# Kernel tuning notes

Hardware: AMD Instinct MI355X
Metric: run time of the kernel (lower is better)

## Reference

```python
import jax, jax.numpy as jnp
import numpy as np

EPS = 1e-7  # keras backend epsilon

def setup_inputs() -> dict:
    key = jax.random.key(0)
    k1, k2, k3 = jax.random.split(key, 3)
    B, L, D, P = 16, 1024, 256, 20
    sent1 = jax.random.normal(k1, (B, L, D), dtype=jnp.float32)
    sent2 = jax.random.normal(k2, (B, L, D), dtype=jnp.float32)
    kernel = jax.random.normal(k3, (P, D), dtype=jnp.float32) * 0.1
    return {"sent1": sent1, "sent2": sent2, "kernel": kernel}

def reference(sent1, sent2, kernel):
    # token norms with keras-style clamping: sqrt(max(sum(x^2), eps))
    n1 = jnp.sqrt(jnp.maximum(jnp.sum(sent1 * sent1, axis=-1), EPS))  # [B,L1]
    n2 = jnp.sqrt(jnp.maximum(jnp.sum(sent2 * sent2, axis=-1), EPS))  # [B,L2]
    # all-pairs cosine matrix via matmul instead of broadcast-multiply-reduce
    dots = jnp.einsum('bld,bmd->blm', sent1, sent2)                    # [B,L1,L2]
    cos = dots / n1[:, :, None] / n2[:, None, :]
    # mean attentive vectors: cosine-weighted sum of sent2, normalized by row sum
    weighted = jnp.einsum('blm,bmd->bld', cos, sent2)                  # [B,L1,D]
    mav = weighted / (jnp.sum(cos, axis=-1, keepdims=True) + EPS)      # [B,L1,D]
    # perspective-weighted cosine between sent1*k and mav*k, fused without [B,L,P,D]
    k2 = kernel * kernel                                               # [P,D]
    num = jnp.einsum('bld,pd->blp', sent1 * mav, k2)                   # sum_d s1*mav*k^2
    nv1 = jnp.sqrt(jnp.maximum(jnp.einsum('bld,pd->blp', sent1 * sent1, k2), EPS))
    nv2 = jnp.sqrt(jnp.maximum(jnp.einsum('bld,pd->blp', mav * mav, k2), EPS))
    return num / nv1 / nv2                                             # [B,L1,P]
```

## Files before the change

### kernel.cpp

```cpp
#include <hip/hip_runtime.h>
#include <math.h>

#define EPS 1e-7f

constexpr int B = 16, L = 1024, D = 256, P = 20;
constexpr int LD = L * D;
constexpr int DD = D * D;

typedef __attribute__((ext_vector_type(8))) _Float16 f16x8;
typedef __attribute__((ext_vector_type(4))) float f32x4;


__device__ inline unsigned short f2h(float x) {
    _Float16 h = (_Float16)x;
    union { _Float16 h; unsigned short u; } c; c.h = h; return c.u;
}
__device__ inline float h2f(unsigned short u) {
    union { unsigned short u; _Float16 h; } c; c.u = u; return (float)c.h;
}

__global__ __launch_bounds__(256) void k_prep2(const float* __restrict__ s2,
                                               float* __restrict__ tp,
                                               unsigned short* __restrict__ CT) {
    __shared__ float tile[32][257];
    __shared__ float wiv[32];
    __shared__ float wsq[32];
    int tid = threadIdx.x;
    int b   = blockIdx.x >> 5, mt = blockIdx.x & 31;
    int m0  = mt * 32;
    {
        int r = tid >> 3, c0 = (tid & 7) * 32;
        const float* gp = s2 + (size_t)b * LD + (size_t)(m0 + r) * D + c0;
        float4 v[8];
#pragma unroll
        for (int q = 0; q < 8; ++q) v[q] = ((const float4*)gp)[q];
#pragma unroll
        for (int q = 0; q < 8; ++q) *(float4*)&tile[r][c0 + q * 4] = v[q];
    }
    __syncthreads();
    {
        int r = tid >> 3, seg = tid & 7;
        float s = 0.f;
#pragma unroll
        for (int k = 0; k < 32; ++k) { float v = tile[r][seg * 32 + k]; s += v * v; }
#pragma unroll
        for (int o = 4; o; o >>= 1) s += __shfl_down(s, o, 8);
        if (seg == 0) {
            float iv = 1.0f / sqrtf(fmaxf(s, EPS));
            wiv[r] = iv;
            wsq[r] = sqrtf(iv);
        }
    }
    __syncthreads();
    {
        int dc = tid;
        float tpart = 0.f;
        union { unsigned short us[32]; uint4 q[4]; } ph;
#pragma unroll
        for (int m = 0; m < 32; ++m) {
            float v = tile[m][dc];
            tpart += v * wiv[m];
            ph.us[m] = f2h(v * wsq[m]);
        }
        tp[(size_t)(mt * B + b) * D + dc] = tpart;
        size_t o = (size_t)b * LD + (size_t)dc * L + m0;
        *(uint4*)(CT + o)      = ph.q[0]; *(uint4*)(CT + o + 8)  = ph.q[1];
        *(uint4*)(CT + o + 16) = ph.q[2]; *(uint4*)(CT + o + 24) = ph.q[3];
    }
}

__global__ __launch_bounds__(256) void k_u(const float* __restrict__ s1,
                                           const float* __restrict__ tp,
                                           float* __restrict__ invU,
                                           unsigned short* __restrict__ s1f) {
    __shared__ float ts[D];
    int tid = threadIdx.x;
    {
        int b0 = (blockIdx.x * 4) >> 10;
        float acc = 0.f;
#pragma unroll
        for (int mc = 0; mc < 32; ++mc)
            acc += tp[(size_t)(mc * B + b0) * D + tid];
        ts[tid] = acc;
    }
    __syncthreads();

    int w = tid >> 6, lane = tid & 63;
    int row = blockIdx.x * 4 + w;
    int dg = lane & 15;

    float4 sv[4];
    float up = 0.f, sq = 0.f;
#pragma unroll
    for (int j = 0; j < 4; ++j) {
        sv[j] = *(const float4*)(s1 + (size_t)row * D + dg * 4 + j * 64);
        float4 tv = *(const float4*)(ts + dg * 4 + j * 64);
        up += sv[j].x * tv.x + sv[j].y * tv.y + sv[j].z * tv.z + sv[j].w * tv.w;
        sq += sv[j].x * sv[j].x + sv[j].y * sv[j].y + sv[j].z * sv[j].z + sv[j].w * sv[j].w;
    }
#pragma unroll
    for (int o = 8; o; o >>= 1) {
        up += __shfl_down(up, o, 16);
        sq += __shfl_down(sq, o, 16);
    }
    if (lane == 0) {
        float n1v = sqrtf(fmaxf(sq, EPS));
        invU[row] = 1.0f / (up + EPS * n1v);
    }
#pragma unroll
    for (int j = 0; j < 4; ++j) {
        ushort4 h4;
        h4.x = f2h(sv[j].x); h4.y = f2h(sv[j].y);
        h4.z = f2h(sv[j].z); h4.w = f2h(sv[j].w);
        *(ushort4*)(s1f + (size_t)row * D + dg * 4 + j * 64) = h4;
    }
}

__global__ __launch_bounds__(256) void k_gram_mfma(const unsigned short* __restrict__ CT,
                                                   float* __restrict__ Gp) {
    __shared__ short As[128 * 72];
    __shared__ short Bs[64 * 72];
    int tid  = threadIdx.x;
    int b    = blockIdx.x >> 5;
    int rem  = blockIdx.x & 31;
    int ti   = rem >> 4;
    int tj   = (rem >> 2) & 3;
    int kc   = rem & 3;
    int wave = tid >> 6, lane = tid & 63;
    int wr   = (wave >> 1) * 64, wcc = (wave & 1) * 32;
    int lr   = lane & 15, lq = lane >> 4;
    int arow = tid >> 1, ahalf = (tid & 1) * 32;
    int brow = tid >> 2, bq = (tid & 3) * 16;

    f32x4 acc[4][2];
#pragma unroll
    for (int i = 0; i < 4; ++i)
#pragma unroll
        for (int j = 0; j < 2; ++j) acc[i][j] = (f32x4){0.f, 0.f, 0.f, 0.f};

#pragma unroll 1
    for (int kb = 0; kb < 4; ++kb) {
        int koff = kc * 256 + kb * 64;
        __syncthreads();
        {
            const unsigned short* ga = CT + (size_t)b * LD + (size_t)(ti * 128 + arow) * L + koff + ahalf;
            uint4 a0 = ((const uint4*)ga)[0], a1 = ((const uint4*)ga)[1];
            uint4 a2 = ((const uint4*)ga)[2], a3 = ((const uint4*)ga)[3];
            const unsigned short* gb = CT + (size_t)b * LD + (size_t)(tj * 64 + brow) * L + koff + bq;
            uint4 b0 = ((const uint4*)gb)[0], b1 = ((const uint4*)gb)[1];
            short* la = &As[arow * 72 + ahalf];
            ((uint4*)la)[0] = a0; ((uint4*)la)[1] = a1;
            ((uint4*)la)[2] = a2; ((uint4*)la)[3] = a3;
            short* lb = &Bs[brow * 72 + bq];
            ((uint4*)lb)[0] = b0; ((uint4*)lb)[1] = b1;
        }
        __syncthreads();
#pragma unroll
        for (int ks = 0; ks < 2; ++ks) {
            f16x8 af[4], bfr[2];
#pragma unroll
            for (int i = 0; i < 4; ++i)
                af[i] = *(const f16x8*)&As[(wr + i * 16 + lr) * 72 + ks * 32 + lq * 8];
#pragma unroll
            for (int j = 0; j < 2; ++j)
                bfr[j] = *(const f16x8*)&Bs[(wcc + j * 16 + lr) * 72 + ks * 32 + lq * 8];
#pragma unroll
            for (int i = 0; i < 4; ++i)
#pragma unroll
                for (int j = 0; j < 2; ++j)
                    acc[i][j] = __builtin_amdgcn_mfma_f32_16x16x32_f16(af[i], bfr[j], acc[i][j], 0, 0, 0);
        }
    }
    float* gout = Gp + ((size_t)(kc * B + b)) * DD;
#pragma unroll
    for (int i = 0; i < 4; ++i)
#pragma unroll
        for (int r = 0; r < 4; ++r) {
            int row = ti * 128 + wr + i * 16 + lq * 4 + r;
#pragma unroll
            for (int j = 0; j < 2; ++j)
                gout[(size_t)row * D + tj * 64 + wcc + j * 16 + lr] = acc[i][j][r];
        }
}

__global__ __launch_bounds__(256) void k_reduceG(const float* __restrict__ Gp,
                                                 unsigned short* __restrict__ Gf) {
    size_t i = ((size_t)blockIdx.x * 256 + threadIdx.x) * 4;
    float4 s = *(const float4*)(Gp + i);
#pragma unroll
    for (int kc = 1; kc < 4; ++kc) {
        float4 a = *(const float4*)(Gp + (size_t)kc * B * DD + i);
        s.x += a.x; s.y += a.y; s.z += a.z; s.w += a.w;
    }
    ushort4 h4;
    h4.x = f2h(s.x); h4.y = f2h(s.y); h4.z = f2h(s.z); h4.w = f2h(s.w);
    *(ushort4*)(Gf + i) = h4;
}

__global__ __launch_bounds__(256) void k_mav_mfma(const unsigned short* __restrict__ s1f,
                                                  const unsigned short* __restrict__ Gf,
                                                  unsigned short* __restrict__ mavh) {
    __shared__ short As[64 * 72];
    __shared__ short Bs[128 * 72];
    int tid  = threadIdx.x;
    int b    = blockIdx.x >> 5;
    int rem  = blockIdx.x & 31;
    int lt   = rem >> 1, nt = rem & 1;
    int l0   = lt * 64, n0 = nt * 128;
    int wave = tid >> 6, lane = tid & 63;
    int wn   = wave * 32;
    int lr   = lane & 15, lq = lane >> 4;
    int arow = tid >> 2, aq = (tid & 3) * 16;
    int brow = tid >> 1, bhalf = (tid & 1) * 32;

    f32x4 acc[4][2];
#pragma unroll
    for (int i = 0; i < 4; ++i)
#pragma unroll
        for (int j = 0; j < 2; ++j) acc[i][j] = (f32x4){0.f, 0.f, 0.f, 0.f};

#pragma unroll 1
    for (int kb = 0; kb < 4; ++kb) {
        int koff = kb * 64;
        __syncthreads();
        {
            const unsigned short* ga = s1f + (size_t)(b * L + l0 + arow) * D + koff + aq;
            uint4 a0 = ((const uint4*)ga)[0], a1 = ((const uint4*)ga)[1];
            const unsigned short* gb = Gf + (size_t)b * DD + (size_t)(n0 + brow) * D + koff + bhalf;
            uint4 b0 = ((const uint4*)gb)[0], b1 = ((const uint4*)gb)[1];
            uint4 b2 = ((const uint4*)gb)[2], b3 = ((const uint4*)gb)[3];
            short* la = &As[arow * 72 + aq];
            ((uint4*)la)[0] = a0; ((uint4*)la)[1] = a1;
            short* lb = &Bs[brow * 72 + bhalf];
            ((uint4*)lb)[0] = b0; ((uint4*)lb)[1] = b1;
            ((uint4*)lb)[2] = b2; ((uint4*)lb)[3] = b3;
        }
        __syncthreads();
#pragma unroll
        for (int ks = 0; ks < 2; ++ks) {
            f16x8 af[4], bfr[2];
#pragma unroll
            for (int i = 0; i < 4; ++i)
                af[i] = *(const f16x8*)&As[(i * 16 + lr) * 72 + ks * 32 + lq * 8];
#pragma unroll
            for (int j = 0; j < 2; ++j)
                bfr[j] = *(const f16x8*)&Bs[(wn + j * 16 + lr) * 72 + ks * 32 + lq * 8];
#pragma unroll
            for (int i = 0; i < 4; ++i)
#pragma unroll
                for (int j = 0; j < 2; ++j)
                    acc[i][j] = __builtin_amdgcn_mfma_f32_16x16x32_f16(af[i], bfr[j], acc[i][j], 0, 0, 0);
        }
    }
#pragma unroll
    for (int i = 0; i < 4; ++i)
#pragma unroll
        for (int r = 0; r < 4; ++r) {
            int l = l0 + i * 16 + lq * 4 + r;
#pragma unroll
            for (int j = 0; j < 2; ++j)
                mavh[(size_t)(b * L + l) * D + n0 + wn + j * 16 + lr] = f2h(acc[i][j][r]);
        }
}

__global__ __launch_bounds__(256) void k_out(const unsigned short* __restrict__ s1f,
                                             const unsigned short* __restrict__ mavh,
                                             const float* __restrict__ invU,
                                             const float* __restrict__ kern,
                                             float* __restrict__ out) {
    __shared__ float k2s[P * D];
    int tid = threadIdx.x;
#pragma unroll
    for (int p = 0; p < P; ++p) {
        float v = kern[p * D + tid];
        k2s[p * D + tid] = v * v;
    }
    __syncthreads();

    int w = tid >> 6, lane = tid & 63;
    int row = blockIdx.x * 4 + w;
    int dg = lane & 15, ps = lane >> 4;

    float4 sm[4], ss[4], mm[4];
#pragma unroll
    for (int j = 0; j < 4; ++j) {
        ushort4 h4 = *(const ushort4*)(s1f + (size_t)row * D + dg * 4 + j * 64);
        ushort4 m4 = *(const ushort4*)(mavh + (size_t)row * D + dg * 4 + j * 64);
        float4 sv, mv;
        sv.x = h2f(h4.x); sv.y = h2f(h4.y); sv.z = h2f(h4.z); sv.w = h2f(h4.w);
        mv.x = h2f(m4.x); mv.y = h2f(m4.y); mv.z = h2f(m4.z); mv.w = h2f(m4.w);
        sm[j].x = sv.x * mv.x; sm[j].y = sv.y * mv.y; sm[j].z = sv.z * mv.z; sm[j].w = sv.w * mv.w;
        ss[j].x = sv.x * sv.x; ss[j].y = sv.y * sv.y; ss[j].z = sv.z * sv.z; ss[j].w = sv.w * sv.w;
        mm[j].x = mv.x * mv.x; mm[j].y = mv.y * mv.y; mm[j].z = mv.z * mv.z; mm[j].w = mv.w * mv.w;
    }
    float sgn = (invU[row] < 0.f) ? -1.f : 1.f;
#pragma unroll
    for (int tI = 0; tI < 5; ++tI) {
        int p = ps + tI * 4;
        float na = 0.f, nb = 0.f, nc = 0.f;
#pragma unroll
        for (int j = 0; j < 4; ++j) {
            float4 kv = *(const float4*)&k2s[p * D + j * 64 + dg * 4];
            na += sm[j].x * kv.x + sm[j].y * kv.y + sm[j].z * kv.z + sm[j].w * kv.w;
            nb += ss[j].x * kv.x + ss[j].y * kv.y + ss[j].z * kv.z + ss[j].w * kv.w;
            nc += mm[j].x * kv.x + mm[j].y * kv.y + mm[j].z * kv.z + mm[j].w * kv.w;
        }
#pragma unroll
        for (int o = 8; o; o >>= 1) {
            na += __shfl_down(na, o, 16);
            nb += __shfl_down(nb, o, 16);
            nc += __shfl_down(nc, o, 16);
        }
        if (dg == 0) {
            out[(size_t)row * P + p] = sgn * na * rsqrtf(fmaxf(nb, EPS)) *
                                       rsqrtf(fmaxf(nc, EPS));
        }
    }
}

extern "C" void kernel_launch(void* const* d_in, const int* in_sizes, int n_in,
                              void* d_out, int out_size, void* d_ws, size_t ws_size,
                              hipStream_t stream) {
    const float* s1   = (const float*)d_in[0];
    const float* s2   = (const float*)d_in[1];
    const float* kern = (const float*)d_in[2];
    float* out = (float*)d_out;
    float* ws  = (float*)d_ws;

    float* tp   = ws;
    float* invU = ws + 131072;
    unsigned short* s1f  = (unsigned short*)(ws + 147456);
    unsigned short* CT   = (unsigned short*)(ws + 2244608);
    unsigned short* Gf   = (unsigned short*)(ws + 4341760);
    float* Gp   = ws + 4866048;
    unsigned short* mavh = (unsigned short*)(ws + 9060352);

    k_prep2<<<512, 256, 0, stream>>>(s2, tp, CT);
    k_u<<<4096, 256, 0, stream>>>(s1, tp, invU, s1f);
    k_gram_mfma<<<512, 256, 0, stream>>>(CT, Gp);
    k_reduceG<<<1024, 256, 0, stream>>>(Gp, Gf);
    k_mav_mfma<<<512, 256, 0, stream>>>(s1f, Gf, mavh);
    k_out<<<4096, 256, 0, stream>>>(s1f, mavh, invU, kern, out);
}
```

Measured before the change: 127.5 us.

## Fuse gram split-K reduction in LDS and merge mav, norm and output kernels

The Gram kernel is retiled to 32x32 output tiles, with its split-K done across the four waves and reduced in shared memory, so the fp32 partial buffer and the separate reduce kernel go away. The s1 conversion and norm kernel, the mav MFMA kernel and the output kernel are merged into one 512-thread block per 64 rows. That block keeps the s1 half-precision tile and the mav tile in LDS and never writes them to global memory. This cuts six launches to three and removes large intermediate traffic, at the cost of heavy LDS use per block and only 256 blocks in the fused kernel, which may limit occupancy.

```diff
diff --git a/kernel.cpp b/kernel.cpp
--- a/kernel.cpp
+++ b/kernel.cpp
@@ -69,251 +69,216 @@
     }
 }
 
-__global__ __launch_bounds__(256) void k_u(const float* __restrict__ s1,
-                                           const float* __restrict__ tp,
-                                           float* __restrict__ invU,
-                                           unsigned short* __restrict__ s1f) {
-    __shared__ float ts[D];
-    int tid = threadIdx.x;
-    {
-        int b0 = (blockIdx.x * 4) >> 10;
-        float acc = 0.f;
-#pragma unroll
-        for (int mc = 0; mc < 32; ++mc)
-            acc += tp[(size_t)(mc * B + b0) * D + tid];
-        ts[tid] = acc;
-    }
-    __syncthreads();
-
-    int w = tid >> 6, lane = tid & 63;
-    int row = blockIdx.x * 4 + w;
-    int dg = lane & 15;
-
-    float4 sv[4];
-    float up = 0.f, sq = 0.f;
-#pragma unroll
-    for (int j = 0; j < 4; ++j) {
-        sv[j] = *(const float4*)(s1 + (size_t)row * D + dg * 4 + j * 64);
-        float4 tv = *(const float4*)(ts + dg * 4 + j * 64);
-        up += sv[j].x * tv.x + sv[j].y * tv.y + sv[j].z * tv.z + sv[j].w * tv.w;
-        sq += sv[j].x * sv[j].x + sv[j].y * sv[j].y + sv[j].z * sv[j].z + sv[j].w * sv[j].w;
-    }
-#pragma unroll
-    for (int o = 8; o; o >>= 1) {
-        up += __shfl_down(up, o, 16);
-        sq += __shfl_down(sq, o, 16);
-    }
-    if (lane == 0) {
-        float n1v = sqrtf(fmaxf(sq, EPS));
-        invU[row] = 1.0f / (up + EPS * n1v);
-    }
-#pragma unroll
-    for (int j = 0; j < 4; ++j) {
-        ushort4 h4;
-        h4.x = f2h(sv[j].x); h4.y = f2h(sv[j].y);
-        h4.z = f2h(sv[j].z); h4.w = f2h(sv[j].w);
-        *(ushort4*)(s1f + (size_t)row * D + dg * 4 + j * 64) = h4;
-    }
-}
-
-__global__ __launch_bounds__(256) void k_gram_mfma(const unsigned short* __restrict__ CT,
-                                                   float* __restrict__ Gp) {
-    __shared__ short As[128 * 72];
-    __shared__ short Bs[64 * 72];
+__global__ __launch_bounds__(256) void k_gram32(const unsigned short* __restrict__ CT,
+                                                unsigned short* __restrict__ Gf) {
+    __shared__ short smem[2 * 32 * 264];
+    short* As = smem;
+    short* Bs = smem + 32 * 264;
     int tid  = threadIdx.x;
-    int b    = blockIdx.x >> 5;
-    int rem  = blockIdx.x & 31;
-    int ti   = rem >> 4;
-    int tj   = (rem >> 2) & 3;
-    int kc   = rem & 3;
+    int b    = blockIdx.x >> 6;
+    int ti   = (blockIdx.x >> 3) & 7;
+    int tj   = blockIdx.x & 7;
     int wave = tid >> 6, lane = tid & 63;
-    int wr   = (wave >> 1) * 64, wcc = (wave & 1) * 32;
     int lr   = lane & 15, lq = lane >> 4;
-    int arow = tid >> 1, ahalf = (tid & 1) * 32;
-    int brow = tid >> 2, bq = (tid & 3) * 16;
-
-    f32x4 acc[4][2];
-#pragma unroll
-    for (int i = 0; i < 4; ++i)
+    int srow = tid >> 3, sseg = (tid & 7) * 32;
+
+    f32x4 acc[2][2];
+#pragma unroll
+    for (int i = 0; i < 2; ++i)
 #pragma unroll
         for (int j = 0; j < 2; ++j) acc[i][j] = (f32x4){0.f, 0.f, 0.f, 0.f};
 
 #pragma unroll 1
     for (int kb = 0; kb < 4; ++kb) {
-        int koff = kc * 256 + kb * 64;
+        int koff = kb * 256;
         __syncthreads();
         {
-            const unsigned short* ga = CT + (size_t)b * LD + (size_t)(ti * 128 + arow) * L + koff + ahalf;
+            const unsigned short* ga = CT + (size_t)b * LD + (size_t)(ti * 32 + srow) * L + koff + sseg;
             uint4 a0 = ((const uint4*)ga)[0], a1 = ((const uint4*)ga)[1];
             uint4 a2 = ((const uint4*)ga)[2], a3 = ((const uint4*)ga)[3];
-            const unsigned short* gb = CT + (size_t)b * LD + (size_t)(tj * 64 + brow) * L + koff + bq;
+            const unsigned short* gb = CT + (size_t)b * LD + (size_t)(tj * 32 + srow) * L + koff + sseg;
             uint4 b0 = ((const uint4*)gb)[0], b1 = ((const uint4*)gb)[1];
-            short* la = &As[arow * 72 + ahalf];
+            uint4 b2 = ((const uint4*)gb)[2], b3 = ((const uint4*)gb)[3];
+            short* la = &As[srow * 264 + sseg];
             ((uint4*)la)[0] = a0; ((uint4*)la)[1] = a1;
             ((uint4*)la)[2] = a2; ((uint4*)la)[3] = a3;
-            short* lb = &Bs[brow * 72 + bq];
+            short* lb = &Bs[srow * 264 + sseg];
             ((uint4*)lb)[0] = b0; ((uint4*)lb)[1] = b1;
+            ((uint4*)lb)[2] = b2; ((uint4*)lb)[3] = b3;
         }
         __syncthreads();
 #pragma unroll
-        for (int ks = 0; ks < 2; ++ks) {
-            f16x8 af[4], bfr[2];
-#pragma unroll
-            for (int i = 0; i < 4; ++i)
-                af[i] = *(const f16x8*)&As[(wr + i * 16 + lr) * 72 + ks * 32 + lq * 8];
+        for (int kk = 0; kk < 2; ++kk) {
+            int ks = wave * 2 + kk;
+            f16x8 af[2], bf[2];
+#pragma unroll
+            for (int i = 0; i < 2; ++i)
+                af[i] = *(const f16x8*)&As[(i * 16 + lr) * 264 + ks * 32 + lq * 8];
 #pragma unroll
             for (int j = 0; j < 2; ++j)
-                bfr[j] = *(const f16x8*)&Bs[(wcc + j * 16 + lr) * 72 + ks * 32 + lq * 8];
-#pragma unroll
-            for (int i = 0; i < 4; ++i)
+                bf[j] = *(const f16x8*)&Bs[(j * 16 + lr) * 264 + ks * 32 + lq * 8];
+#pragma unroll
+            for (int i = 0; i < 2; ++i)
 #pragma unroll
                 for (int j = 0; j < 2; ++j)
-                    acc[i][j] = __builtin_amdgcn_mfma_f32_16x16x32_f16(af[i], bfr[j], acc[i][j], 0, 0, 0);
-        }
-    }
-    float* gout = Gp + ((size_t)(kc * B + b)) * DD;
-#pragma unroll
-    for (int i = 0; i < 4; ++i)
-#pragma unroll
-        for (int r = 0; r < 4; ++r) {
-            int row = ti * 128 + wr + i * 16 + lq * 4 + r;
-#pragma unroll
-            for (int j = 0; j < 2; ++j)
-                gout[(size_t)row * D + tj * 64 + wcc + j * 16 + lr] = acc[i][j][r];
-        }
-}
-
-__global__ __launch_bounds__(256) void k_reduceG(const float* __restrict__ Gp,
-                                                 unsigned short* __restrict__ Gf) {
-    size_t i = ((size_t)blockIdx.x * 256 + threadIdx.x) * 4;
-    float4 s = *(const float4*)(Gp + i);
-#pragma unroll
-    for (int kc = 1; kc < 4; ++kc) {
-        float4 a = *(const float4*)(Gp + (size_t)kc * B * DD + i);
-        s.x += a.x; s.y += a.y; s.z += a.z; s.w += a.w;
-    }
-    ushort4 h4;
-    h4.x = f2h(s.x); h4.y = f2h(s.y); h4.z = f2h(s.z); h4.w = f2h(s.w);
-    *(ushort4*)(Gf + i) = h4;
-}
-
-__global__ __launch_bounds__(256) void k_mav_mfma(const unsigned short* __restrict__ s1f,
-                                                  const unsigned short* __restrict__ Gf,
-                                                  unsigned short* __restrict__ mavh) {
-    __shared__ short As[64 * 72];
-    __shared__ short Bs[128 * 72];
+                    acc[i][j] = __builtin_amdgcn_mfma_f32_16x16x32_f16(af[i], bf[j], acc[i][j], 0, 0, 0);
+        }
+    }
+    __syncthreads();
+    float* red = (float*)smem;
+#pragma unroll
+    for (int i = 0; i < 2; ++i)
+#pragma unroll
+        for (int j = 0; j < 2; ++j)
+#pragma unroll
+            for (int r = 0; r < 4; ++r) {
+                int row = i * 16 + lq * 4 + r, col = j * 16 + lr;
+                red[wave * 1056 + row * 33 + col] = acc[i][j][r];
+            }
+    __syncthreads();
+#pragma unroll
+    for (int k = 0; k < 4; ++k) {
+        int e = tid + k * 256;
+        int row = e >> 5, col = e & 31;
+        float s = red[row * 33 + col] + red[1056 + row * 33 + col] +
+                  red[2112 + row * 33 + col] + red[3168 + row * 33 + col];
+        Gf[(size_t)b * DD + (size_t)(ti * 32 + row) * D + tj * 32 + col] = f2h(s);
+    }
+}
+
+__global__ __launch_bounds__(512) void k_mav_out(const float* __restrict__ s1,
+                                                 const float* __restrict__ tp,
+                                                 const unsigned short* __restrict__ Gf,
+                                                 const float* __restrict__ kern,
+                                                 float* __restrict__ out) {
+    __shared__ short As[64 * 264];
+    __shared__ short Bs[64 * 264];
+    __shared__ short Ms[64 * 264];
+    __shared__ float ts[D];
+    __shared__ float sgnS[64];
     int tid  = threadIdx.x;
-    int b    = blockIdx.x >> 5;
-    int rem  = blockIdx.x & 31;
-    int lt   = rem >> 1, nt = rem & 1;
-    int l0   = lt * 64, n0 = nt * 128;
+    int b    = blockIdx.x >> 4, lt = blockIdx.x & 15;
+    int l0   = lt * 64;
     int wave = tid >> 6, lane = tid & 63;
-    int wn   = wave * 32;
     int lr   = lane & 15, lq = lane >> 4;
-    int arow = tid >> 2, aq = (tid & 3) * 16;
-    int brow = tid >> 1, bhalf = (tid & 1) * 32;
-
-    f32x4 acc[4][2];
-#pragma unroll
-    for (int i = 0; i < 4; ++i)
-#pragma unroll
-        for (int j = 0; j < 2; ++j) acc[i][j] = (f32x4){0.f, 0.f, 0.f, 0.f};
-
+
+    if (tid < 256) {
+        float a = 0.f;
+#pragma unroll
+        for (int mc = 0; mc < 32; ++mc) a += tp[(size_t)(mc * B + b) * D + tid];
+        ts[tid] = a;
+    }
+    __syncthreads();
+
+    {
+        int r = tid >> 3, seg = tid & 7;
+        const float* gp = s1 + (size_t)(b * L + l0 + r) * D + seg * 32;
+        float up = 0.f, sq = 0.f;
+        union { unsigned short us[32]; uint4 q[4]; } hb;
+#pragma unroll
+        for (int q8 = 0; q8 < 8; ++q8) {
+            float4 v = ((const float4*)gp)[q8];
+            int td = seg * 32 + q8 * 4;
+            up += v.x * ts[td] + v.y * ts[td + 1] + v.z * ts[td + 2] + v.w * ts[td + 3];
+            sq += v.x * v.x + v.y * v.y + v.z * v.z + v.w * v.w;
+            hb.us[q8 * 4 + 0] = f2h(v.x); hb.us[q8 * 4 + 1] = f2h(v.y);
+            hb.us[q8 * 4 + 2] = f2h(v.z); hb.us[q8 * 4 + 3] = f2h(v.w);
+        }
+        short* la = &As[r * 264 + seg * 32];
+        ((uint4*)la)[0] = hb.q[0]; ((uint4*)la)[1] = hb.q[1];
+        ((uint4*)la)[2] = hb.q[2]; ((uint4*)la)[3] = hb.q[3];
+#pragma unroll
+        for (int o = 4; o; o >>= 1) { up += __shfl_down(up, o, 8); sq += __shfl_down(sq, o, 8); }
+        if (seg == 0) {
+            float n1v = sqrtf(fmaxf(sq, EPS));
+            sgnS[r] = up + EPS * n1v;
+        }
+    }
+
+    int wlr = (wave >> 2) * 32;
+    int wnc = (wave & 3) * 16;
 #pragma unroll 1
-    for (int kb = 0; kb < 4; ++kb) {
-        int koff = kb * 64;
+    for (int nh = 0; nh < 4; ++nh) {
         __syncthreads();
         {
-            const unsigned short* ga = s1f + (size_t)(b * L + l0 + arow) * D + koff + aq;
-            uint4 a0 = ((const uint4*)ga)[0], a1 = ((const uint4*)ga)[1];
-            const unsigned short* gb = Gf + (size_t)b * DD + (size_t)(n0 + brow) * D + koff + bhalf;
+            int r = tid >> 3, seg = (tid & 7) * 32;
+            const unsigned short* gb = Gf + (size_t)b * DD + (size_t)(nh * 64 + r) * D + seg;
             uint4 b0 = ((const uint4*)gb)[0], b1 = ((const uint4*)gb)[1];
             uint4 b2 = ((const uint4*)gb)[2], b3 = ((const uint4*)gb)[3];
-            short* la = &As[arow * 72 + aq];
-            ((uint4*)la)[0] = a0; ((uint4*)la)[1] = a1;
-            short* lb = &Bs[brow * 72 + bhalf];
+            short* lb = &Bs[r * 264 + seg];
             ((uint4*)lb)[0] = b0; ((uint4*)lb)[1] = b1;
             ((uint4*)lb)[2] = b2; ((uint4*)lb)[3] = b3;
         }
         __syncthreads();
-#pragma unroll
-        for (int ks = 0; ks < 2; ++ks) {
-            f16x8 af[4], bfr[2];
-#pragma unroll
-            for (int i = 0; i < 4; ++i)
-                af[i] = *(const f16x8*)&As[(i * 16 + lr) * 72 + ks * 32 + lq * 8];
-#pragma unroll
-            for (int j = 0; j < 2; ++j)
-                bfr[j] = *(const f16x8*)&Bs[(wn + j * 16 + lr) * 72 + ks * 32 + lq * 8];
-#pragma unroll
-            for (int i = 0; i < 4; ++i)
-#pragma unroll
-                for (int j = 0; j < 2; ++j)
-                    acc[i][j] = __builtin_amdgcn_mfma_f32_16x16x32_f16(af[i], bfr[j], acc[i][j], 0, 0, 0);
-        }
-    }
-#pragma unroll
-    for (int i = 0; i < 4; ++i)
-#pragma unroll
-        for (int r = 0; r < 4; ++r) {
-            int l = l0 + i * 16 + lq * 4 + r;
-#pragma unroll
-            for (int j = 0; j < 2; ++j)
-                mavh[(size_t)(b * L + l) * D + n0 + wn + j * 16 + lr] = f2h(acc[i][j][r]);
-        }
-}
-
-__global__ __launch_bounds__(256) void k_out(const unsigned short* __restrict__ s1f,
-                                             const unsigned short* __restrict__ mavh,
-                                             const float* __restrict__ invU,
-                                             const float* __restrict__ kern,
-                                             float* __restrict__ out) {
-    __shared__ float k2s[P * D];
-    int tid = threadIdx.x;
-#pragma unroll
-    for (int p = 0; p < P; ++p) {
-        float v = kern[p * D + tid];
-        k2s[p * D + tid] = v * v;
-    }
-    __syncthreads();
-
-    int w = tid >> 6, lane = tid & 63;
-    int row = blockIdx.x * 4 + w;
+        f32x4 acc[2];
+        acc[0] = (f32x4){0.f, 0.f, 0.f, 0.f};
+        acc[1] = (f32x4){0.f, 0.f, 0.f, 0.f};
+#pragma unroll
+        for (int ks = 0; ks < 8; ++ks) {
+            f16x8 af0 = *(const f16x8*)&As[(wlr + lr) * 264 + ks * 32 + lq * 8];
+            f16x8 af1 = *(const f16x8*)&As[(wlr + 16 + lr) * 264 + ks * 32 + lq * 8];
+            f16x8 bf  = *(const f16x8*)&Bs[(wnc + lr) * 264 + ks * 32 + lq * 8];
+            acc[0] = __builtin_amdgcn_mfma_f32_16x16x32_f16(af0, bf, acc[0], 0, 0, 0);
+            acc[1] = __builtin_amdgcn_mfma_f32_16x16x32_f16(af1, bf, acc[1], 0, 0, 0);
+        }
+#pragma unroll
+        for (int i = 0; i < 2; ++i)
+#pragma unroll
+            for (int r4 = 0; r4 < 4; ++r4)
+                Ms[(wlr + i * 16 + lq * 4 + r4) * 264 + nh * 64 + wnc + lr] = f2h(acc[i][r4]);
+    }
+    __syncthreads();
+
+    float* k2s = (float*)Bs;
+    {
+        int d = tid & 255, ph = tid >> 8;
+#pragma unroll
+        for (int i = 0; i < 10; ++i) {
+            int p = i * 2 + ph;
+            float v = kern[p * D + d];
+            k2s[p * 264 + d] = v * v;
+        }
+    }
+    __syncthreads();
+
     int dg = lane & 15, ps = lane >> 4;
-
-    float4 sm[4], ss[4], mm[4];
-#pragma unroll
-    for (int j = 0; j < 4; ++j) {
-        ushort4 h4 = *(const ushort4*)(s1f + (size_t)row * D + dg * 4 + j * 64);
-        ushort4 m4 = *(const ushort4*)(mavh + (size_t)row * D + dg * 4 + j * 64);
-        float4 sv, mv;
-        sv.x = h2f(h4.x); sv.y = h2f(h4.y); sv.z = h2f(h4.z); sv.w = h2f(h4.w);
-        mv.x = h2f(m4.x); mv.y = h2f(m4.y); mv.z = h2f(m4.z); mv.w = h2f(m4.w);
-        sm[j].x = sv.x * mv.x; sm[j].y = sv.y * mv.y; sm[j].z = sv.z * mv.z; sm[j].w = sv.w * mv.w;
-        ss[j].x = sv.x * sv.x; ss[j].y = sv.y * sv.y; ss[j].z = sv.z * sv.z; ss[j].w = sv.w * sv.w;
-        mm[j].x = mv.x * mv.x; mm[j].y = mv.y * mv.y; mm[j].z = mv.z * mv.z; mm[j].w = mv.w * mv.w;
-    }
-    float sgn = (invU[row] < 0.f) ? -1.f : 1.f;
-#pragma unroll
-    for (int tI = 0; tI < 5; ++tI) {
-        int p = ps + tI * 4;
-        float na = 0.f, nb = 0.f, nc = 0.f;
+#pragma unroll 1
+    for (int rl = 0; rl < 8; ++rl) {
+        int l = wave * 8 + rl;
+        float4 sm[4], ss[4], mm[4];
 #pragma unroll
         for (int j = 0; j < 4; ++j) {
-            float4 kv = *(const float4*)&k2s[p * D + j * 64 + dg * 4];
-            na += sm[j].x * kv.x + sm[j].y * kv.y + sm[j].z * kv.z + sm[j].w * kv.w;
-            nb += ss[j].x * kv.x + ss[j].y * kv.y + ss[j].z * kv.z + ss[j].w * kv.w;
-            nc += mm[j].x * kv.x + mm[j].y * kv.y + mm[j].z * kv.z + mm[j].w * kv.w;
-        }
-#pragma unroll
-        for (int o = 8; o; o >>= 1) {
-            na += __shfl_down(na, o, 16);
-            nb += __shfl_down(nb, o, 16);
-            nc += __shfl_down(nc, o, 16);
-        }
-        if (dg == 0) {
-            out[(size_t)row * P + p] = sgn * na * rsqrtf(fmaxf(nb, EPS)) *
-                                       rsqrtf(fmaxf(nc, EPS));
+            ushort4 h4 = *(const ushort4*)&As[l * 264 + dg * 4 + j * 64];
+            ushort4 m4 = *(const ushort4*)&Ms[l * 264 + dg * 4 + j * 64];
+            float4 sv, mv;
+            sv.x = h2f(h4.x); sv.y = h2f(h4.y); sv.z = h2f(h4.z); sv.w = h2f(h4.w);
+            mv.x = h2f(m4.x); mv.y = h2f(m4.y); mv.z = h2f(m4.z); mv.w = h2f(m4.w);
+            sm[j].x = sv.x * mv.x; sm[j].y = sv.y * mv.y; sm[j].z = sv.z * mv.z; sm[j].w = sv.w * mv.w;
+            ss[j].x = sv.x * sv.x; ss[j].y = sv.y * sv.y; ss[j].z = sv.z * sv.z; ss[j].w = sv.w * sv.w;
+            mm[j].x = mv.x * mv.x; mm[j].y = mv.y * mv.y; mm[j].z = mv.z * mv.z; mm[j].w = mv.w * mv.w;
+        }
+        float sgn = (sgnS[l] < 0.f) ? -1.f : 1.f;
+#pragma unroll
+        for (int tI = 0; tI < 5; ++tI) {
+            int p = ps + tI * 4;
+            float na = 0.f, nb = 0.f, nc = 0.f;
+#pragma unroll
+            for (int j = 0; j < 4; ++j) {
+                float4 kv = *(const float4*)&k2s[p * 264 + j * 64 + dg * 4];
+                na += sm[j].x * kv.x + sm[j].y * kv.y + sm[j].z * kv.z + sm[j].w * kv.w;
+                nb += ss[j].x * kv.x + ss[j].y * kv.y + ss[j].z * kv.z + ss[j].w * kv.w;
+                nc += mm[j].x * kv.x + mm[j].y * kv.y + mm[j].z * kv.z + mm[j].w * kv.w;
+            }
+#pragma unroll
+            for (int o = 8; o; o >>= 1) {
+                na += __shfl_down(na, o, 16);
+                nb += __shfl_down(nb, o, 16);
+                nc += __shfl_down(nc, o, 16);
+            }
+            if (dg == 0) {
+                out[(size_t)(b * L + l0 + l) * P + p] =
+                    sgn * na * rsqrtf(fmaxf(nb, EPS)) * rsqrtf(fmaxf(nc, EPS));
+            }
         }
     }
 }
@@ -327,18 +292,11 @@
     float* out = (float*)d_out;
     float* ws  = (float*)d_ws;
 
-    float* tp   = ws;
-    float* invU = ws + 131072;
-    unsigned short* s1f  = (unsigned short*)(ws + 147456);
-    unsigned short* CT   = (unsigned short*)(ws + 2244608);
-    unsigned short* Gf   = (unsigned short*)(ws + 4341760);
-    float* Gp   = ws + 4866048;
-    unsigned short* mavh = (unsigned short*)(ws + 9060352);
+    float* tp = ws;
+    unsigned short* CT = (unsigned short*)(ws + 131072);
+    unsigned short* Gf = (unsigned short*)(ws + 2228224);
 
     k_prep2<<<512, 256, 0, stream>>>(s2, tp, CT);
-    k_u<<<4096, 256, 0, stream>>>(s1, tp, invU, s1f);
-    k_gram_mfma<<<512, 256, 0, stream>>>(CT, Gp);
-    k_reduceG<<<1024, 256, 0, stream>>>(Gp, Gf);
-    k_mav_mfma<<<512, 256, 0, stream>>>(s1f, Gf, mavh);
-    k_out<<<4096, 256, 0, stream>>>(s1f, mavh, invU, kern, out);
-}
+    k_gram32<<<1024, 256, 0, stream>>>(CT, Gf);
+    k_mav_out<<<256, 512, 0, stream>>>(s1, tp, Gf, kern, out);
+}
```

Result: faster. 122.6 us (-3.8%).
